# Kernel tuning notes

Hardware: AMD Instinct MI355X
Metric: run time of the kernel (lower is better)

The kernel has to match this reference:

```python
import jax, jax.numpy as jnp
import numpy as np
from jax import lax

B, W_LEN, N_E = 16, 32, 1024
CS = 12
KS = [3, 5, 7]
D = (len(KS) * W_LEN - sum(KS) + len(KS)) * CS  # 1008
HID1, HID2 = 40, 10
DN = ('NCHW', 'OIHW', 'NCHW')


def setup_inputs() -> dict:
    key = jax.random.key(0)
    ks = jax.random.split(key, 16)
    x = jax.random.normal(ks[0], (B, W_LEN, N_E), dtype=jnp.float32)
    # adjacency: nonneg, column-normalized (A / A.sum(0)), tiled per batch
    A0 = jax.random.uniform(ks[1], (N_E, N_E), dtype=jnp.float32)
    A0 = A0 / jnp.sum(A0, axis=0, keepdims=True)
    A = jnp.broadcast_to(A0, (B, N_E, N_E))
    s = 0.05
    inp = {
        'x': x, 'A': A,
        'W1': jax.random.normal(ks[2], (CS, 1, 1, KS[0]), jnp.float32) * s,
        'b1': jnp.zeros((CS,), jnp.float32),
        'W2': jax.random.normal(ks[3], (CS, 1, 1, KS[1]), jnp.float32) * s,
        'b2': jnp.zeros((CS,), jnp.float32),
        'W3': jax.random.normal(ks[4], (CS, 1, 1, KS[2]), jnp.float32) * s,
        'b3': jnp.zeros((CS,), jnp.float32),
        'Wg1': jax.random.normal(ks[5], (D, HID1), jnp.float32) * s,
        'bg1': jnp.zeros((HID1,), jnp.float32),
        'Wg2': jax.random.normal(ks[6], (HID1, HID2), jnp.float32) * s,
        'bg2': jnp.zeros((HID2,), jnp.float32),
        'Wg3': jax.random.normal(ks[7], (HID2, 1), jnp.float32) * s,
        'bg3': jnp.zeros((1,), jnp.float32),
    }
    return inp


def _branch(c, Wc, bc):
    # c: [B,1,N,W]; Wc: [CS,1,1,k] -> [B,CS,N,Lk] -> [B,N,CS*Lk]
    y = lax.conv_general_dilated(c, Wc, (1, 1), 'VALID', dimension_numbers=DN)
    y = y + bc[None, :, None, None]
    y = jnp.transpose(y, (0, 2, 1, 3))  # [B,N,CS,Lk]
    return y.reshape(B, N_E, -1)


def _dense_gcn(x, adj, Wg, bg):
    # DenseGCNConv: xW, adj+I, sym-normalize, propagate, bias
    x = x @ Wg
    adj = adj + jnp.eye(N_E, dtype=adj.dtype)[None]
    deg = jnp.clip(jnp.sum(adj, axis=-1), 1.0, None)
    dis = lax.rsqrt(deg)
    adj = dis[..., None] * adj * dis[..., None, :]
    return jnp.einsum('bij,bjd->bid', adj, x) + bg


def reference(x, A, W1, b1, W2, b2, W3, b3, Wg1, bg1, Wg2, bg2, Wg3, bg3):
    c = jnp.transpose(x, (0, 2, 1))[:, None, :, :]  # [B,1,N,W]
    a1 = _branch(c, W1, b1)
    a2 = _branch(c, W2, b2)
    a3 = _branch(c, W3, b3)
    x_conv = jax.nn.relu(jnp.concatenate([a1, a2, a3], axis=2))  # [B,N,D]
    x1 = jax.nn.relu(_dense_gcn(x_conv, A, Wg1, bg1))
    x2 = jax.nn.relu(_dense_gcn(x1, A, Wg2, bg2))
    x3 = _dense_gcn(x2, A, Wg3, bg3)
    return jnp.squeeze(x3, axis=-1)  # [B,N]
```

## Files before the change

kernel.cpp:

```cpp
#include <hip/hip_runtime.h>

#define NB_B 16
#define NN   1024
#define NW   32
#define NCS  12
#define NH1  40
#define NH2  10

#define OFF_DIS  0
#define OFF_G0   1024
#define OFF_X1   (OFF_G0 + NN*NB_B*NH1)
#define OFF_G1   (OFF_X1 + NN*NB_B*NH1)
#define OFF_G2   (OFF_G1 + NN*NB_B*NH2)
#define OFF_SCR  (OFF_G2 + NN*NB_B)

__global__ __launch_bounds__(256) void k_dis(const float* __restrict__ A0,
                                             float* __restrict__ dis) {
    int i = blockIdx.x;
    const float* row = A0 + (size_t)i * NN;
    float s = 0.f;
    for (int j = threadIdx.x; j < NN; j += 256) s += row[j];
#pragma unroll
    for (int off = 32; off > 0; off >>= 1) s += __shfl_down(s, off);
    __shared__ float red[4];
    int lane = threadIdx.x & 63, wv = threadIdx.x >> 6;
    if (lane == 0) red[wv] = s;
    __syncthreads();
    if (threadIdx.x == 0) {
        float deg = 1.f + red[0] + red[1] + red[2] + red[3];
        dis[i] = rsqrtf(fmaxf(deg, 1.f));
    }
}

template <int KSZ, int LK, int DBASE, int BR>
__device__ __forceinline__ void feat_body(const float* __restrict__ x,
                                          const float* __restrict__ Wc,
                                          const float* __restrict__ bc,
                                          const float* __restrict__ Wg1,
                                          float* __restrict__ P,
                                          float (*xs)[256], float (*xc)[256]) {
    int tid = threadIdx.x;
    int n0 = blockIdx.x * 256;
    int b  = blockIdx.y;
    for (int idx = tid; idx < NW * 256; idx += 256) {
        int w = idx >> 8, j = idx & 255;
        xs[w][j] = x[((size_t)b * NW + w) * NN + n0 + j];
    }
    __syncthreads();
    int hg = tid & 3, ng = tid >> 2;
    int h0 = hg * 10;
    float acc[4][10];
#pragma unroll
    for (int a = 0; a < 4; ++a)
#pragma unroll
        for (int u = 0; u < 10; ++u) acc[a][u] = 0.f;

    for (int cs = 0; cs < NCS; ++cs) {
        if (cs) __syncthreads();
        float wk[KSZ];
#pragma unroll
        for (int t = 0; t < KSZ; ++t) wk[t] = Wc[cs * KSZ + t];
        float bb = bc[cs];
        for (int l = 0; l < LK; ++l) {
            float s = bb;
#pragma unroll
            for (int t = 0; t < KSZ; ++t) s += xs[l + t][tid] * wk[t];
            xc[l][tid] = fmaxf(s, 0.f);
        }
        __syncthreads();
        const float* wrow = Wg1 + (size_t)(DBASE + cs * LK) * NH1 + h0;
        for (int l = 0; l < LK; ++l) {
            float4 xv = *(const float4*)&xc[l][ng * 4];
            const float* wr = wrow + l * NH1;
#pragma unroll
            for (int u = 0; u < 10; ++u) {
                float wv = wr[u];
                acc[0][u] = fmaf(xv.x, wv, acc[0][u]);
                acc[1][u] = fmaf(xv.y, wv, acc[1][u]);
                acc[2][u] = fmaf(xv.z, wv, acc[2][u]);
                acc[3][u] = fmaf(xv.w, wv, acc[3][u]);
            }
        }
    }
#pragma unroll
    for (int nn = 0; nn < 4; ++nn) {
        int n = n0 + ng * 4 + nn;
        float* dst = P + (((size_t)BR * NN + n) * NB_B + b) * NH1 + h0;
#pragma unroll
        for (int u = 0; u < 10; ++u) dst[u] = acc[nn][u];
    }
}

__global__ __launch_bounds__(256) void k_feat(
    const float* __restrict__ x, const float* __restrict__ W1,
    const float* __restrict__ b1, const float* __restrict__ W2,
    const float* __restrict__ b2, const float* __restrict__ W3,
    const float* __restrict__ b3, const float* __restrict__ Wg1,
    float* __restrict__ P) {
    __shared__ float xs[NW][256];
    __shared__ float xc[30][256];
    int br = blockIdx.z;
    if (br == 0)      feat_body<3, 30, 0,   0>(x, W1, b1, Wg1, P, xs, xc);
    else if (br == 1) feat_body<5, 28, 360, 1>(x, W2, b2, Wg1, P, xs, xc);
    else              feat_body<7, 26, 696, 2>(x, W3, b3, Wg1, P, xs, xc);
}

__global__ __launch_bounds__(256) void k_combine(const float* __restrict__ P,
                                                 const float* __restrict__ dis,
                                                 float* __restrict__ G0) {
    int t = blockIdx.x * 256 + threadIdx.x;
    int n = t / 160;
    const float4* p = (const float4*)P;
    float4 a = p[t];
    float4 b = p[t + NN * 160];
    float4 c = p[t + 2 * NN * 160];
    float d = dis[n];
    float4 o;
    o.x = d * (a.x + b.x + c.x);
    o.y = d * (a.y + b.y + c.y);
    o.z = d * (a.z + b.z + c.z);
    o.w = d * (a.w + b.w + c.w);
    ((float4*)G0)[t] = o;
}

__global__ __launch_bounds__(256) void k_prop1(const float* __restrict__ A0,
                                               const float* __restrict__ G0,
                                               const float* __restrict__ dis,
                                               const float* __restrict__ bg1,
                                               float* __restrict__ X1) {
    __shared__ float As[32][68];
    __shared__ float Bs[32][68];
    int tid = threadIdx.x;
    int n0 = blockIdx.x * 64;
    int i0 = blockIdx.y * 64;
    int tx = tid & 15, ty = tid >> 4;
    float acc[4][4] = {};
    for (int kc = 0; kc < NN; kc += 32) {
#pragma unroll
        for (int v = 0; v < 2; ++v) {
            int fid = tid + v * 256;
            int r = fid >> 3, c4 = (fid & 7) * 4;
            float4 a = *(const float4*)&A0[(size_t)(i0 + r) * NN + kc + c4];
            As[c4 + 0][r] = a.x; As[c4 + 1][r] = a.y;
            As[c4 + 2][r] = a.z; As[c4 + 3][r] = a.w;
            int r2 = fid >> 4, c42 = (fid & 15) * 4;
            *(float4*)&Bs[r2][c42] =
                *(const float4*)&G0[(size_t)(kc + r2) * 640 + n0 + c42];
        }
        __syncthreads();
#pragma unroll
        for (int kk = 0; kk < 32; ++kk) {
            float4 av = *(const float4*)&As[kk][ty * 4];
            float4 bv = *(const float4*)&Bs[kk][tx * 4];
            acc[0][0] = fmaf(av.x, bv.x, acc[0][0]);
            acc[0][1] = fmaf(av.x, bv.y, acc[0][1]);
            acc[0][2] = fmaf(av.x, bv.z, acc[0][2]);
            acc[0][3] = fmaf(av.x, bv.w, acc[0][3]);
            acc[1][0] = fmaf(av.y, bv.x, acc[1][0]);
            acc[1][1] = fmaf(av.y, bv.y, acc[1][1]);
            acc[1][2] = fmaf(av.y, bv.z, acc[1][2]);
            acc[1][3] = fmaf(av.y, bv.w, acc[1][3]);
            acc[2][0] = fmaf(av.z, bv.x, acc[2][0]);
            acc[2][1] = fmaf(av.z, bv.y, acc[2][1]);
            acc[2][2] = fmaf(av.z, bv.z, acc[2][2]);
            acc[2][3] = fmaf(av.z, bv.w, acc[2][3]);
            acc[3][0] = fmaf(av.w, bv.x, acc[3][0]);
            acc[3][1] = fmaf(av.w, bv.y, acc[3][1]);
            acc[3][2] = fmaf(av.w, bv.z, acc[3][2]);
            acc[3][3] = fmaf(av.w, bv.w, acc[3][3]);
        }
        __syncthreads();
    }
    int col = n0 + tx * 4;
    int h0 = col % 40;
    float4 bv = *(const float4*)&bg1[h0];
#pragma unroll
    for (int iy = 0; iy < 4; ++iy) {
        int i = i0 + ty * 4 + iy;
        float di = dis[i];
        float4 g = *(const float4*)&G0[(size_t)i * 640 + col];
        float4 o;
        o.x = fmaxf(di * (acc[iy][0] + g.x) + bv.x, 0.f);
        o.y = fmaxf(di * (acc[iy][1] + g.y) + bv.y, 0.f);
        o.z = fmaxf(di * (acc[iy][2] + g.z) + bv.z, 0.f);
        o.w = fmaxf(di * (acc[iy][3] + g.w) + bv.w, 0.f);
        *(float4*)&X1[(size_t)i * 640 + col] = o;
    }
}

__global__ __launch_bounds__(256) void k_x1w2(const float* __restrict__ X1,
                                              const float* __restrict__ Wg2,
                                              const float* __restrict__ dis,
                                              float* __restrict__ G1) {
    __shared__ float w2[NH1 * NH2];
    int tid = threadIdx.x;
    for (int idx = tid; idx < NH1 * NH2; idx += 256) w2[idx] = Wg2[idx];
    __syncthreads();
    int t = blockIdx.x * 256 + tid;
    int i = t >> 4, b = t & 15;
    const float* xr = X1 + (size_t)i * 640 + b * 40;
    float di = dis[i];
    float o[10];
#pragma unroll
    for (int m = 0; m < 10; ++m) o[m] = 0.f;
#pragma unroll
    for (int h4 = 0; h4 < 10; ++h4) {
        float4 xv = *(const float4*)&xr[h4 * 4];
#pragma unroll
        for (int m = 0; m < 10; ++m) {
            o[m] = fmaf(xv.x, w2[(h4 * 4 + 0) * 10 + m], o[m]);
            o[m] = fmaf(xv.y, w2[(h4 * 4 + 1) * 10 + m], o[m]);
            o[m] = fmaf(xv.z, w2[(h4 * 4 + 2) * 10 + m], o[m]);
            o[m] = fmaf(xv.w, w2[(h4 * 4 + 3) * 10 + m], o[m]);
        }
    }
    float* dst = G1 + (size_t)i * 160 + b * 10;
#pragma unroll
    for (int m = 0; m < 10; ++m) dst[m] = di * o[m];
}

__global__ __launch_bounds__(256) void k_prop2(const float* __restrict__ A0,
                                               const float* __restrict__ G1,
                                               float* __restrict__ P2) {
    __shared__ float As[32][68];
    __shared__ float Gs[32][164];
    int tid = threadIdx.x;
    int kb = blockIdx.x * 128;
    int i0 = blockIdx.y * 64;
    int cg = tid & 15, ig = tid >> 4;
    float acc[4][10] = {};
    for (int kc = 0; kc < 128; kc += 32) {
#pragma unroll
        for (int v = 0; v < 2; ++v) {
            int fid = tid + v * 256;
            int r = fid >> 3, c4 = (fid & 7) * 4;
            float4 a = *(const float4*)&A0[(size_t)(i0 + r) * NN + kb + kc + c4];
            As[c4 + 0][r] = a.x; As[c4 + 1][r] = a.y;
            As[c4 + 2][r] = a.z; As[c4 + 3][r] = a.w;
        }
#pragma unroll
        for (int v = 0; v < 5; ++v) {
            int fid = tid + v * 256;
            int r = fid / 40, c4 = (fid % 40) * 4;
            *(float4*)&Gs[r][c4] =
                *(const float4*)&G1[(size_t)(kb + kc + r) * 160 + c4];
        }
        __syncthreads();
#pragma unroll
        for (int kk = 0; kk < 32; ++kk) {
            float4 av = *(const float4*)&As[kk][ig * 4];
#pragma unroll
            for (int u = 0; u < 10; ++u) {
                float g = Gs[kk][cg + 16 * u];
                acc[0][u] = fmaf(av.x, g, acc[0][u]);
                acc[1][u] = fmaf(av.y, g, acc[1][u]);
                acc[2][u] = fmaf(av.z, g, acc[2][u]);
                acc[3][u] = fmaf(av.w, g, acc[3][u]);
            }
        }
        __syncthreads();
    }
#pragma unroll
    for (int iy = 0; iy < 4; ++iy) {
        float* dst = P2 + ((size_t)blockIdx.x * NN + i0 + ig * 4 + iy) * 160;
#pragma unroll
        for (int u = 0; u < 10; ++u) dst[cg + 16 * u] = acc[iy][u];
    }
}

__global__ __launch_bounds__(256) void k_red2(const float* __restrict__ P2,
                                              const float* __restrict__ G1,
                                              const float* __restrict__ dis,
                                              const float* __restrict__ bg2,
                                              const float* __restrict__ Wg3,
                                              float* __restrict__ G2) {
    int t = blockIdx.x * 256 + threadIdx.x;
    int i = t >> 4, b = t & 15;
    float s[10];
#pragma unroll
    for (int m = 0; m < 10; ++m) s[m] = G1[(size_t)i * 160 + b * 10 + m];
    for (int kc = 0; kc < 8; ++kc) {
        const float* p = P2 + (size_t)kc * NN * 160 + (size_t)i * 160 + b * 10;
#pragma unroll
        for (int m = 0; m < 10; ++m) s[m] += p[m];
    }
    float di = dis[i];
    float g2 = 0.f;
#pragma unroll
    for (int m = 0; m < 10; ++m) {
        float x2 = fmaxf(di * s[m] + bg2[m], 0.f);
        g2 = fmaf(x2, Wg3[m], g2);
    }
    G2[(size_t)i * 16 + b] = di * g2;
}

__global__ __launch_bounds__(256) void k_prop3(const float* __restrict__ A0,
                                               const float* __restrict__ G2,
                                               float* __restrict__ P3) {
    __shared__ float As[32][132];
    __shared__ float G2s[128][16];
    int tid = threadIdx.x;
    int kb = blockIdx.x * 128;
    int i0 = blockIdx.y * 128;
#pragma unroll
    for (int v = 0; v < 2; ++v) {
        int fid = tid + v * 256;
        int r = fid >> 2, c4 = (fid & 3) * 4;
        *(float4*)&G2s[r][c4] = *(const float4*)&G2[(size_t)(kb + r) * 16 + c4];
    }
    int il = tid >> 1, c0 = (tid & 1) * 8;
    float acc[8] = {};
    for (int jc = 0; jc < 128; jc += 32) {
#pragma unroll
        for (int v = 0; v < 4; ++v) {
            int fid = tid + v * 256;
            int r = fid >> 3, c4 = (fid & 7) * 4;
            float4 a = *(const float4*)&A0[(size_t)(i0 + r) * NN + kb + jc + c4];
            As[c4 + 0][r] = a.x; As[c4 + 1][r] = a.y;
            As[c4 + 2][r] = a.z; As[c4 + 3][r] = a.w;
        }
        __syncthreads();
#pragma unroll
        for (int kk = 0; kk < 32; ++kk) {
            float a = As[kk][il];
            float4 g0 = *(const float4*)&G2s[jc + kk][c0];
            float4 g1 = *(const float4*)&G2s[jc + kk][c0 + 4];
            acc[0] = fmaf(a, g0.x, acc[0]);
            acc[1] = fmaf(a, g0.y, acc[1]);
            acc[2] = fmaf(a, g0.z, acc[2]);
            acc[3] = fmaf(a, g0.w, acc[3]);
            acc[4] = fmaf(a, g1.x, acc[4]);
            acc[5] = fmaf(a, g1.y, acc[5]);
            acc[6] = fmaf(a, g1.z, acc[6]);
            acc[7] = fmaf(a, g1.w, acc[7]);
        }
        __syncthreads();
    }
    float* dst = P3 + (size_t)blockIdx.x * NN * 16 + (size_t)(i0 + il) * 16 + c0;
#pragma unroll
    for (int u = 0; u < 8; ++u) dst[u] = acc[u];
}

__global__ __launch_bounds__(256) void k_red3(const float* __restrict__ P3,
                                              const float* __restrict__ G2,
                                              const float* __restrict__ dis,
                                              const float* __restrict__ bg3,
                                              float* __restrict__ out) {
    int t = blockIdx.x * 256 + threadIdx.x;
    int i = t >> 4, b = t & 15;
    float s = G2[(size_t)i * 16 + b];
#pragma unroll
    for (int kc = 0; kc < 8; ++kc) s += P3[(size_t)kc * NN * 16 + i * 16 + b];
    out[(size_t)b * NN + i] = dis[i] * s + bg3[0];
}

extern "C" void kernel_launch(void* const* d_in, const int* in_sizes, int n_in,
                              void* d_out, int out_size, void* d_ws,
                              size_t ws_size, hipStream_t stream) {
    (void)in_sizes; (void)n_in; (void)out_size; (void)ws_size;
    const float* x   = (const float*)d_in[0];
    const float* A   = (const float*)d_in[1];
    const float* W1  = (const float*)d_in[2];
    const float* b1  = (const float*)d_in[3];
    const float* W2  = (const float*)d_in[4];
    const float* b2  = (const float*)d_in[5];
    const float* W3  = (const float*)d_in[6];
    const float* b3  = (const float*)d_in[7];
    const float* Wg1 = (const float*)d_in[8];
    const float* bg1 = (const float*)d_in[9];
    const float* Wg2 = (const float*)d_in[10];
    const float* bg2 = (const float*)d_in[11];
    const float* Wg3 = (const float*)d_in[12];
    const float* bg3 = (const float*)d_in[13];
    float* ws  = (float*)d_ws;
    float* dis = ws + OFF_DIS;
    float* G0  = ws + OFF_G0;
    float* X1  = ws + OFF_X1;
    float* G1  = ws + OFF_G1;
    float* G2  = ws + OFF_G2;
    float* SCR = ws + OFF_SCR;
    float* out = (float*)d_out;

    k_dis<<<NN, 256, 0, stream>>>(A, dis);
    k_feat<<<dim3(4, 16, 3), 256, 0, stream>>>(x, W1, b1, W2, b2, W3, b3, Wg1, SCR);
    k_combine<<<640, 256, 0, stream>>>(SCR, dis, G0);
    k_prop1<<<dim3(10, 16), 256, 0, stream>>>(A, G0, dis, bg1, X1);
    k_x1w2<<<64, 256, 0, stream>>>(X1, Wg2, dis, G1);
    k_prop2<<<dim3(8, 16), 256, 0, stream>>>(A, G1, SCR);
    k_red2<<<64, 256, 0, stream>>>(SCR, G1, dis, bg2, Wg3, G2);
    k_prop3<<<dim3(8, 8), 256, 0, stream>>>(A, G2, SCR);
    k_red3<<<64, 256, 0, stream>>>(SCR, G2, dis, bg3, out);
}
```

Baseline: 264.8 us.

## Register-resident conv features, transposed G0, and split-K first propagation

The feature kernel now keeps each node's 32-sample window in registers, with each wave computing 10 hidden outputs. This drops the shared-memory staging and the barriers, and the grid grows fourfold. Its output is stored feature-major, so the combine step writes G0 transposed and the first propagation GEMM loads both operands with the same transposed pattern. That GEMM is split three ways along K to get 480 blocks instead of 160, and a new finalize kernel sums the partials and applies the self-loop, scaling, bias and ReLU. The cost is an extra kernel launch and extra partial-sum traffic, and the finalize kernel reads G0T with strided, uncoalesced accesses.

```diff
diff --git a/kernel.cpp b/kernel.cpp
--- a/kernel.cpp
+++ b/kernel.cpp
@@ -8,8 +8,8 @@
 #define NH2  10
 
 #define OFF_DIS  0
-#define OFF_G0   1024
-#define OFF_X1   (OFF_G0 + NN*NB_B*NH1)
+#define OFF_G0T  1024
+#define OFF_X1   (OFF_G0T + NN*NB_B*NH1)
 #define OFF_G1   (OFF_X1 + NN*NB_B*NH1)
 #define OFF_G2   (OFF_G1 + NN*NB_B*NH2)
 #define OFF_SCR  (OFF_G2 + NN*NB_B)
@@ -37,58 +37,40 @@
                                           const float* __restrict__ Wc,
                                           const float* __restrict__ bc,
                                           const float* __restrict__ Wg1,
-                                          float* __restrict__ P,
-                                          float (*xs)[256], float (*xc)[256]) {
-    int tid = threadIdx.x;
-    int n0 = blockIdx.x * 256;
-    int b  = blockIdx.y;
-    for (int idx = tid; idx < NW * 256; idx += 256) {
-        int w = idx >> 8, j = idx & 255;
-        xs[w][j] = x[((size_t)b * NW + w) * NN + n0 + j];
-    }
-    __syncthreads();
-    int hg = tid & 3, ng = tid >> 2;
-    int h0 = hg * 10;
-    float acc[4][10];
-#pragma unroll
-    for (int a = 0; a < 4; ++a)
-#pragma unroll
-        for (int u = 0; u < 10; ++u) acc[a][u] = 0.f;
-
+                                          float* __restrict__ Pf) {
+    int lane = threadIdx.x & 63;
+    int hq = __builtin_amdgcn_readfirstlane(threadIdx.x >> 6);
+    int n = blockIdx.x * 64 + lane;
+    int b = blockIdx.y;
+
+    float xs[NW];
+#pragma unroll
+    for (int w = 0; w < NW; ++w) xs[w] = x[((size_t)b * NW + w) * NN + n];
+
+    float acc[10];
+#pragma unroll
+    for (int u = 0; u < 10; ++u) acc[u] = 0.f;
+
+    const float* wg = Wg1 + (size_t)DBASE * NH1 + hq * 10;
     for (int cs = 0; cs < NCS; ++cs) {
-        if (cs) __syncthreads();
         float wk[KSZ];
 #pragma unroll
         for (int t = 0; t < KSZ; ++t) wk[t] = Wc[cs * KSZ + t];
         float bb = bc[cs];
+#pragma unroll
         for (int l = 0; l < LK; ++l) {
             float s = bb;
 #pragma unroll
-            for (int t = 0; t < KSZ; ++t) s += xs[l + t][tid] * wk[t];
-            xc[l][tid] = fmaxf(s, 0.f);
-        }
-        __syncthreads();
-        const float* wrow = Wg1 + (size_t)(DBASE + cs * LK) * NH1 + h0;
-        for (int l = 0; l < LK; ++l) {
-            float4 xv = *(const float4*)&xc[l][ng * 4];
-            const float* wr = wrow + l * NH1;
-#pragma unroll
-            for (int u = 0; u < 10; ++u) {
-                float wv = wr[u];
-                acc[0][u] = fmaf(xv.x, wv, acc[0][u]);
-                acc[1][u] = fmaf(xv.y, wv, acc[1][u]);
-                acc[2][u] = fmaf(xv.z, wv, acc[2][u]);
-                acc[3][u] = fmaf(xv.w, wv, acc[3][u]);
-            }
-        }
-    }
-#pragma unroll
-    for (int nn = 0; nn < 4; ++nn) {
-        int n = n0 + ng * 4 + nn;
-        float* dst = P + (((size_t)BR * NN + n) * NB_B + b) * NH1 + h0;
-#pragma unroll
-        for (int u = 0; u < 10; ++u) dst[u] = acc[nn][u];
-    }
+            for (int t = 0; t < KSZ; ++t) s = fmaf(xs[l + t], wk[t], s);
+            s = fmaxf(s, 0.f);
+            const float* wr = wg + (size_t)(cs * LK + l) * NH1;
+#pragma unroll
+            for (int u = 0; u < 10; ++u) acc[u] = fmaf(s, wr[u], acc[u]);
+        }
+    }
+    float* dst = Pf + (((size_t)BR * NB_B + b) * NH1 + hq * 10) * NN + n;
+#pragma unroll
+    for (int u = 0; u < 10; ++u) dst[(size_t)u * NN] = acc[u];
 }
 
 __global__ __launch_bounds__(256) void k_feat(
@@ -96,46 +78,44 @@
     const float* __restrict__ b1, const float* __restrict__ W2,
     const float* __restrict__ b2, const float* __restrict__ W3,
     const float* __restrict__ b3, const float* __restrict__ Wg1,
-    float* __restrict__ P) {
-    __shared__ float xs[NW][256];
-    __shared__ float xc[30][256];
+    float* __restrict__ Pf) {
     int br = blockIdx.z;
-    if (br == 0)      feat_body<3, 30, 0,   0>(x, W1, b1, Wg1, P, xs, xc);
-    else if (br == 1) feat_body<5, 28, 360, 1>(x, W2, b2, Wg1, P, xs, xc);
-    else              feat_body<7, 26, 696, 2>(x, W3, b3, Wg1, P, xs, xc);
-}
-
-__global__ __launch_bounds__(256) void k_combine(const float* __restrict__ P,
+    if (br == 0)      feat_body<3, 30, 0,   0>(x, W1, b1, Wg1, Pf);
+    else if (br == 1) feat_body<5, 28, 360, 1>(x, W2, b2, Wg1, Pf);
+    else              feat_body<7, 26, 696, 2>(x, W3, b3, Wg1, Pf);
+}
+
+__global__ __launch_bounds__(256) void k_combine(const float* __restrict__ Pf,
                                                  const float* __restrict__ dis,
-                                                 float* __restrict__ G0) {
-    int t = blockIdx.x * 256 + threadIdx.x;
-    int n = t / 160;
-    const float4* p = (const float4*)P;
-    float4 a = p[t];
-    float4 b = p[t + NN * 160];
-    float4 c = p[t + 2 * NN * 160];
-    float d = dis[n];
-    float4 o;
-    o.x = d * (a.x + b.x + c.x);
-    o.y = d * (a.y + b.y + c.y);
-    o.z = d * (a.z + b.z + c.z);
-    o.w = d * (a.w + b.w + c.w);
-    ((float4*)G0)[t] = o;
-}
-
-__global__ __launch_bounds__(256) void k_prop1(const float* __restrict__ A0,
-                                               const float* __restrict__ G0,
-                                               const float* __restrict__ dis,
-                                               const float* __restrict__ bg1,
-                                               float* __restrict__ X1) {
+                                                 float* __restrict__ G0T) {
+    int c = blockIdx.x;
+    const float* p = Pf + (size_t)c * NN;
+    float* dst = G0T + (size_t)c * NN;
+#pragma unroll
+    for (int k = 0; k < 4; ++k) {
+        int n = k * 256 + threadIdx.x;
+        float v = p[n] + p[(size_t)NB_B * NH1 * NN + n] +
+                  p[(size_t)2 * NB_B * NH1 * NN + n];
+        dst[n] = dis[n] * v;
+    }
+}
+
+__global__ __launch_bounds__(256) void k_prop1s(const float* __restrict__ A0,
+                                                const float* __restrict__ G0T,
+                                                float* __restrict__ P1a,
+                                                float* __restrict__ P1b) {
     __shared__ float As[32][68];
     __shared__ float Bs[32][68];
     int tid = threadIdx.x;
     int n0 = blockIdx.x * 64;
     int i0 = blockIdx.y * 64;
+    int z  = blockIdx.z;
+    int kc0 = z * 352;
+    int kc1 = (z == 2) ? NN : kc0 + 352;
+    float* P = (z == 0) ? P1a : (P1b + (size_t)(z - 1) * NN * 640);
     int tx = tid & 15, ty = tid >> 4;
     float acc[4][4] = {};
-    for (int kc = 0; kc < NN; kc += 32) {
+    for (int kc = kc0; kc < kc1; kc += 32) {
 #pragma unroll
         for (int v = 0; v < 2; ++v) {
             int fid = tid + v * 256;
@@ -143,9 +123,9 @@
             float4 a = *(const float4*)&A0[(size_t)(i0 + r) * NN + kc + c4];
             As[c4 + 0][r] = a.x; As[c4 + 1][r] = a.y;
             As[c4 + 2][r] = a.z; As[c4 + 3][r] = a.w;
-            int r2 = fid >> 4, c42 = (fid & 15) * 4;
-            *(float4*)&Bs[r2][c42] =
-                *(const float4*)&G0[(size_t)(kc + r2) * 640 + n0 + c42];
+            float4 g = *(const float4*)&G0T[(size_t)(n0 + r) * NN + kc + c4];
+            Bs[c4 + 0][r] = g.x; Bs[c4 + 1][r] = g.y;
+            Bs[c4 + 2][r] = g.z; Bs[c4 + 3][r] = g.w;
         }
         __syncthreads();
 #pragma unroll
@@ -172,20 +152,39 @@
         __syncthreads();
     }
     int col = n0 + tx * 4;
-    int h0 = col % 40;
-    float4 bv = *(const float4*)&bg1[h0];
 #pragma unroll
     for (int iy = 0; iy < 4; ++iy) {
         int i = i0 + ty * 4 + iy;
-        float di = dis[i];
-        float4 g = *(const float4*)&G0[(size_t)i * 640 + col];
         float4 o;
-        o.x = fmaxf(di * (acc[iy][0] + g.x) + bv.x, 0.f);
-        o.y = fmaxf(di * (acc[iy][1] + g.y) + bv.y, 0.f);
-        o.z = fmaxf(di * (acc[iy][2] + g.z) + bv.z, 0.f);
-        o.w = fmaxf(di * (acc[iy][3] + g.w) + bv.w, 0.f);
-        *(float4*)&X1[(size_t)i * 640 + col] = o;
-    }
+        o.x = acc[iy][0]; o.y = acc[iy][1]; o.z = acc[iy][2]; o.w = acc[iy][3];
+        *(float4*)&P[(size_t)i * 640 + col] = o;
+    }
+}
+
+__global__ __launch_bounds__(256) void k_fin1(float* __restrict__ P1a,
+                                              const float* __restrict__ P1b,
+                                              const float* __restrict__ G0T,
+                                              const float* __restrict__ dis,
+                                              const float* __restrict__ bg1) {
+    int f4 = blockIdx.x * 256 + threadIdx.x;
+    int i = f4 / 160;
+    int c4 = (f4 % 160) * 4;
+    float4 a = ((const float4*)P1a)[f4];
+    float4 b = ((const float4*)P1b)[f4];
+    float4 c = ((const float4*)P1b)[f4 + NN * 160];
+    float g0 = G0T[(size_t)(c4 + 0) * NN + i];
+    float g1 = G0T[(size_t)(c4 + 1) * NN + i];
+    float g2 = G0T[(size_t)(c4 + 2) * NN + i];
+    float g3 = G0T[(size_t)(c4 + 3) * NN + i];
+    int h0 = c4 % 40;
+    float4 bv = *(const float4*)&bg1[h0];
+    float di = dis[i];
+    float4 o;
+    o.x = fmaxf(di * (a.x + b.x + c.x + g0) + bv.x, 0.f);
+    o.y = fmaxf(di * (a.y + b.y + c.y + g1) + bv.y, 0.f);
+    o.z = fmaxf(di * (a.z + b.z + c.z + g2) + bv.z, 0.f);
+    o.w = fmaxf(di * (a.w + b.w + c.w + g3) + bv.w, 0.f);
+    ((float4*)P1a)[f4] = o;
 }
 
 __global__ __launch_bounds__(256) void k_x1w2(const float* __restrict__ X1,
@@ -374,7 +373,7 @@
     const float* bg3 = (const float*)d_in[13];
     float* ws  = (float*)d_ws;
     float* dis = ws + OFF_DIS;
-    float* G0  = ws + OFF_G0;
+    float* G0T = ws + OFF_G0T;
     float* X1  = ws + OFF_X1;
     float* G1  = ws + OFF_G1;
     float* G2  = ws + OFF_G2;
@@ -382,9 +381,10 @@
     float* out = (float*)d_out;
 
     k_dis<<<NN, 256, 0, stream>>>(A, dis);
-    k_feat<<<dim3(4, 16, 3), 256, 0, stream>>>(x, W1, b1, W2, b2, W3, b3, Wg1, SCR);
-    k_combine<<<640, 256, 0, stream>>>(SCR, dis, G0);
-    k_prop1<<<dim3(10, 16), 256, 0, stream>>>(A, G0, dis, bg1, X1);
+    k_feat<<<dim3(16, 16, 3), 256, 0, stream>>>(x, W1, b1, W2, b2, W3, b3, Wg1, SCR);
+    k_combine<<<640, 256, 0, stream>>>(SCR, dis, G0T);
+    k_prop1s<<<dim3(10, 16, 3), 256, 0, stream>>>(A, G0T, X1, SCR);
+    k_fin1<<<640, 256, 0, stream>>>(X1, SCR, G0T, dis, bg1);
     k_x1w2<<<64, 256, 0, stream>>>(X1, Wg2, dis, G1);
     k_prop2<<<dim3(8, 16), 256, 0, stream>>>(A, G1, SCR);
     k_red2<<<64, 256, 0, stream>>>(SCR, G1, dis, bg2, Wg3, G2);
```

Result: faster. 219.9 us (-17.0%).
